# Kernel tuning notes

Hardware: AMD Instinct MI355X
Metric: run time of the kernel (lower is better)

## Reference

```python
import jax, jax.numpy as jnp
import numpy as np

TOP_K = 2
SCALING = 2.0  # LoRA alpha/rank scaling


def setup_inputs() -> dict:
    key = jax.random.key(0)
    ks = jax.random.split(key, 10)
    B, S, H, I, E, R = 1, 512, 2048, 1024, 8, 16
    w = 1.0 / np.sqrt(H)
    inp = {
        "x": jax.random.normal(ks[0], (B, S, H), jnp.float32),
        "gate_weight": jax.random.normal(ks[1], (E, H), jnp.float32) * w,
        "gate_lora_A": jax.random.normal(ks[2], (R, H), jnp.float32) * 0.02,
        "gate_lora_B": jax.random.normal(ks[3], (E, R), jnp.float32) * 0.02,
        "gate_up_proj": jax.random.normal(ks[4], (E, H, 2 * I), jnp.float32) * w,
        "down_proj": jax.random.normal(ks[5], (E, I, H), jnp.float32) * (1.0 / np.sqrt(I)),
        "gup_lora_A": jax.random.normal(ks[6], (E, R, H), jnp.float32) * 0.02,
        "gup_lora_B": jax.random.normal(ks[7], (E, 2 * I, R), jnp.float32) * 0.02,
        "down_lora_A": jax.random.normal(ks[8], (E, R, I), jnp.float32) * 0.02,
        "down_lora_B": jax.random.normal(ks[9], (E, H, R), jnp.float32) * 0.02,
    }
    return inp


def reference(x, gate_weight, gate_lora_A, gate_lora_B, gate_up_proj, down_proj,
              gup_lora_A, gup_lora_B, down_lora_A, down_lora_B):
    B, S, H = x.shape
    xf = x.reshape(-1, H)  # [T, H]

    # ---- router (base weight + LoRA delta) ----
    gate_delta = SCALING * (gate_lora_B @ gate_lora_A)  # [E, H]
    router_logits = xf @ gate_weight.T + xf @ gate_delta.T  # [T, E]
    probs = jax.nn.softmax(router_logits.astype(jnp.float32), axis=-1)
    routing_weights, selected = jax.lax.top_k(probs, TOP_K)  # [T, K]
    routing_weights = routing_weights / routing_weights.sum(-1, keepdims=True)  # norm_topk_prob
    routing_weights = routing_weights.astype(xf.dtype)

    # ---- expert MLP: compute all experts, combine top-k ----
    # (math identical to sparse scatter/grouped-GEMM dispatch for selected experts)
    gup = jnp.einsum('th,eho->teo', xf, gate_up_proj)  # [T, E, 2I]
    gup = gup + SCALING * jnp.einsum('ter,eor->teo',
                                     jnp.einsum('th,erh->ter', xf, gup_lora_A),
                                     gup_lora_B)
    gates, h = jnp.split(gup, 2, axis=-1)
    h = jax.nn.silu(gates) * h  # [T, E, I]

    out = jnp.einsum('tei,eih->teh', h, down_proj)  # [T, E, H]
    out = out + SCALING * jnp.einsum('ter,ehr->teh',
                                     jnp.einsum('tei,eri->ter', h, down_lora_A),
                                     down_lora_B)

    # gather the top-k expert outputs and combine with routing weights
    out_sel = jnp.take_along_axis(out, selected[:, :, None], axis=1)  # [T, K, H]
    y = jnp.einsum('tkh,tk->th', out_sel, routing_weights)
    return y.reshape(B, S, H)
```

## Files before the change

kernel.cpp:

```cpp
#include <hip/hip_runtime.h>


typedef short  s16x8 __attribute__((ext_vector_type(8)));
typedef float  f32x4 __attribute__((ext_vector_type(4)));
typedef unsigned short u16x8 __attribute__((ext_vector_type(8)));

__device__ __forceinline__ unsigned short f2bf(float f) {
  unsigned u = __builtin_bit_cast(unsigned, f);
  u += 0x7fffu + ((u >> 16) & 1u);
  return (unsigned short)(u >> 16);
}

#define PIPE_BARRIER() asm volatile("s_waitcnt lgkmcnt(0)\n\ts_barrier" ::: "memory")

#define OFF_CNT    0u
#define OFF_TER1A  256u
#define OFF_TER2   262400u
#define ZERO_SPAN  327936u
#define OFF_LIST   327936u
#define OFF_PW     344320u
#define OFF_WG     348416u
#define OFF_XBF    413952u
#define OFF_H      2511104u
#define OFF_OSEL   4608256u

__global__ void k_gatecomb(const float* __restrict__ gw, const float* __restrict__ gA,
                           const float* __restrict__ gB, float* __restrict__ Wg) {
  int idx = blockIdx.x * 256 + threadIdx.x;
  int e = idx >> 11, h = idx & 2047;
  float acc = gw[idx];
#pragma unroll
  for (int r = 0; r < 16; ++r)
    acc += 2.0f * gB[e * 16 + r] * gA[r * 2048 + h];
  Wg[idx] = acc;
}

__global__ void k_router(const float* __restrict__ x, const float* __restrict__ Wg,
                         int* __restrict__ cnt, int* __restrict__ list,
                         float* __restrict__ pw, unsigned short* __restrict__ xbf) {
  int t = blockIdx.x, tid = threadIdx.x;
  __shared__ float xs[2048];
  __shared__ float logits[8];
  for (int i = tid; i < 2048; i += 256) xs[i] = x[(size_t)t * 2048 + i];
  __syncthreads();
  {
    u16x8 o;
#pragma unroll
    for (int j = 0; j < 8; ++j) o[j] = f2bf(xs[tid * 8 + j]);
    *(u16x8*)(xbf + (size_t)t * 2048 + tid * 8) = o;
  }
  int e = tid >> 5, l = tid & 31;
  float s = 0.f;
  for (int h = l; h < 2048; h += 32) s += xs[h] * Wg[e * 2048 + h];
#pragma unroll
  for (int off = 16; off >= 1; off >>= 1) s += __shfl_down(s, off, 32);
  if (l == 0) logits[e] = s;
  __syncthreads();
  if (tid == 0) {
    float m = logits[0];
#pragma unroll
    for (int i = 1; i < 8; ++i) m = fmaxf(m, logits[i]);
    float ex[8];
#pragma unroll
    for (int i = 0; i < 8; ++i) ex[i] = __expf(logits[i] - m);
    int e1 = 0; float v1 = ex[0];
#pragma unroll
    for (int i = 1; i < 8; ++i) if (ex[i] > v1) { v1 = ex[i]; e1 = i; }
    int e2 = -1; float v2 = -1.f;
#pragma unroll
    for (int i = 0; i < 8; ++i) if (i != e1 && ex[i] > v2) { v2 = ex[i]; e2 = i; }
    float inv = 1.f / (v1 + v2);
    int p1 = 2 * t, p2 = 2 * t + 1;
    pw[p1] = v1 * inv;
    pw[p2] = v2 * inv;
    int s1 = atomicAdd(&cnt[e1], 1); list[e1 * 512 + s1] = p1;
    int s2 = atomicAdd(&cnt[e2], 1); list[e2 * 512 + s2] = p2;
  }
}

__global__ __launch_bounds__(512) void k_ter1all(
    const unsigned short* __restrict__ xbf, const float* __restrict__ gupA,
    float* __restrict__ ter1all) {
  int trow = blockIdx.x, kcc = blockIdx.y;
  int tid = threadIdx.x;
  __shared__ unsigned short Ap[2][64 * 64];
  __shared__ unsigned short Bp[2][128 * 64];
  const int k0b = kcc * 512;

  int rowA = tid >> 3, k16A = tid & 7;
  const unsigned short* aSrc = xbf + (size_t)(trow * 64 + rowA) * 2048 + k0b + k16A * 8;
  int aOff = rowA * 64 + ((k16A * 8) ^ ((rowA & 7) << 3));

  const float* bSrc[2]; int bOff[2];
#pragma unroll
  for (int s = 0; s < 2; ++s) {
    int slot = tid + s * 512;
    int er = slot >> 3, kg = slot & 7;
    bSrc[s] = gupA + (size_t)er * 2048 + k0b + kg * 8;
    bOff[s] = er * 64 + ((kg * 8) ^ ((er & 7) << 3));
  }
  int lane = tid & 63, wv = tid >> 6;
  int lr = lane & 15, lh = lane >> 4;

  uint4 apre; float4 bpre[2][2];
#define TA_ISSUE(T) { int kk = (T) * 64;                                   \
    apre = *(const uint4*)(aSrc + kk);                                     \
    _Pragma("unroll") for (int s = 0; s < 2; ++s) {                        \
      bpre[s][0] = *(const float4*)(bSrc[s] + kk);                         \
      bpre[s][1] = *(const float4*)(bSrc[s] + kk + 4); } }

  f32x4 acc[4] = {};
  TA_ISSUE(0);
  for (int t = 0; t < 8; ++t) {
    int buf = t & 1;
    *(uint4*)&Ap[buf][aOff] = apre;
#pragma unroll
    for (int s = 0; s < 2; ++s) {
      u16x8 o;
      o[0]=f2bf(bpre[s][0].x); o[1]=f2bf(bpre[s][0].y); o[2]=f2bf(bpre[s][0].z); o[3]=f2bf(bpre[s][0].w);
      o[4]=f2bf(bpre[s][1].x); o[5]=f2bf(bpre[s][1].y); o[6]=f2bf(bpre[s][1].z); o[7]=f2bf(bpre[s][1].w);
      *(u16x8*)&Bp[buf][bOff[s]] = o;
    }
    __syncthreads();
    if (t < 7) TA_ISSUE(t + 1);
#pragma unroll
    for (int ks = 0; ks < 64; ks += 32) {
      int kb = ks + lh * 8;
      int bc = wv * 16 + lr;
      s16x8 b = *(const s16x8*)&Bp[buf][bc * 64 + (kb ^ ((bc & 7) << 3))];
#pragma unroll
      for (int fr = 0; fr < 4; ++fr) {
        int ar = fr * 16 + lr;
        s16x8 a = *(const s16x8*)&Ap[buf][ar * 64 + (kb ^ ((ar & 7) << 3))];
        acc[fr] = __builtin_amdgcn_mfma_f32_16x16x32_bf16(a, b, acc[fr], 0, 0, 0);
      }
    }
    __syncthreads();
  }
#undef TA_ISSUE
#pragma unroll
  for (int fr = 0; fr < 4; ++fr)
#pragma unroll
    for (int j = 0; j < 4; ++j) {
      int tok = trow * 64 + fr * 16 + lh * 4 + j;
      atomicAdd(&ter1all[tok * 128 + wv * 16 + lr], acc[fr][j]);
    }
}

__global__ __launch_bounds__(512) void k_gemm1(
    const unsigned short* __restrict__ xbf, const float* __restrict__ gup,
    const float* __restrict__ gupB, const float* __restrict__ ter1all,
    const int* __restrict__ cnt, const int* __restrict__ list,
    unsigned short* __restrict__ h) {
  const int ct = blockIdx.x;
  const int st = blockIdx.y;
  const int e  = blockIdx.z;
  const int n = cnt[e];
  if (st * 128 >= n) return;
  const int tid = threadIdx.x;

  __shared__ unsigned short Ap[2][128 * 64];
  __shared__ unsigned short Bp[2][128 * 64];

  const int c0 = ct * 64;

  const unsigned short *aSrc0, *aSrc1;
  int aOff0, aOff1;
  {
    int row = tid >> 3, k16 = tid & 7;
    int p = list[e * 512 + min(st * 128 + row, n - 1)];
    aSrc0 = xbf + (size_t)(p >> 1) * 2048 + k16 * 8;
    aOff0 = row * 64 + ((k16 * 8) ^ ((row & 7) << 3));
    int slot = tid + 512;
    row = slot >> 3; k16 = slot & 7;
    p = list[e * 512 + min(st * 128 + row, n - 1)];
    aSrc1 = xbf + (size_t)(p >> 1) * 2048 + k16 * 8;
    aOff1 = row * 64 + ((k16 * 8) ^ ((row & 7) << 3));
  }
  const int bcol = tid & 127, kgrp = tid >> 7;
  const int gcg = (bcol < 64) ? (c0 + bcol) : (1024 + c0 + bcol - 64);
  const float* bSrc = gup + (size_t)e * 2048 * 2048 + (size_t)(kgrp * 16) * 2048 + gcg;
  const int sw = (bcol & 7) << 3;
  const int bOff0 = bcol * 64 + ((kgrp * 16) ^ sw);
  const int bOff1 = bcol * 64 + ((kgrp * 16 + 8) ^ sw);

  const int lane = tid & 63, wv = tid >> 6;
  const int lr = lane & 15, lh = lane >> 4;
  const int wr = wv >> 1, ni = wv & 1;

  uint4 a0A, a1A, a0B, a1B;
  float bA[16], bB[16];

#define G1_LOAD(SUF, T) {                                        \
    const int kk = (T) * 64;                                     \
    a0##SUF = *(const uint4*)(aSrc0 + kk);                       \
    a1##SUF = *(const uint4*)(aSrc1 + kk);                       \
    _Pragma("unroll") for (int j = 0; j < 16; ++j)               \
      b##SUF[j] = bSrc[(size_t)(kk + j) * 2048]; }

#define G1_BODY(BUF, SUF, NXT) {                                               \
    *(uint4*)&Ap[BUF][aOff0] = a0##SUF;                                        \
    *(uint4*)&Ap[BUF][aOff1] = a1##SUF;                                        \
    { u16x8 o0, o1;                                                            \
      _Pragma("unroll") for (int j = 0; j < 8; ++j) {                          \
        o0[j] = f2bf(b##SUF[j]); o1[j] = f2bf(b##SUF[j + 8]); }                \
      *(u16x8*)&Bp[BUF][bOff0] = o0;                                           \
      *(u16x8*)&Bp[BUF][bOff1] = o1; }                                         \
    PIPE_BARRIER();                                                            \
    if ((NXT) < 32) G1_LOAD(SUF, NXT);                                         \
    _Pragma("unroll") for (int ks = 0; ks < 64; ks += 32) {                    \
      int kb = ks + lh * 8;                                                    \
      s16x8 af[2], bg[2], bu[2];                                               \
      _Pragma("unroll") for (int q = 0; q < 2; ++q) {                          \
        int ar = wr * 32 + q * 16 + lr;                                        \
        af[q] = *(const s16x8*)&Ap[BUF][ar * 64 + (kb ^ ((ar & 7) << 3))];     \
      }                                                                        \
      _Pragma("unroll") for (int r = 0; r < 2; ++r) {                          \
        int bc = ni * 32 + r * 16 + lr;                                        \
        bg[r] = *(const s16x8*)&Bp[BUF][bc * 64 + (kb ^ ((bc & 7) << 3))];     \
        bu[r] = *(const s16x8*)&Bp[BUF][(bc + 64) * 64 + (kb ^ ((bc & 7) << 3))]; \
      }                                                                        \
      _Pragma("unroll") for (int q = 0; q < 2; ++q)                            \
        _Pragma("unroll") for (int r = 0; r < 2; ++r) {                        \
          accg[q][r] = __builtin_amdgcn_mfma_f32_16x16x32_bf16(af[q], bg[r], accg[q][r], 0, 0, 0); \
          accu[q][r] = __builtin_amdgcn_mfma_f32_16x16x32_bf16(af[q], bu[r], accu[q][r], 0, 0, 0); \
        }                                                                      \
    } }

  f32x4 accg[2][2] = {}, accu[2][2] = {};
  G1_LOAD(A, 0);
  G1_LOAD(B, 1);
  for (int tt = 0; tt < 32; tt += 2) {
    G1_BODY(0, A, tt + 2);
    G1_BODY(1, B, tt + 3);
  }
#undef G1_LOAD
#undef G1_BODY

  __syncthreads();
  float* tlds = (float*)&Ap[0][0];
  for (int idx = tid; idx < 2048; idx += 512) {
    int row = idx >> 4, c = idx & 15;
    int p = list[e * 512 + min(st * 128 + row, n - 1)];
    tlds[idx] = ter1all[(size_t)(p >> 1) * 128 + e * 16 + c];
  }
  __syncthreads();
#pragma unroll
  for (int r = 0; r < 2; ++r) {
    int gc = c0 + ni * 32 + r * 16 + lr;
    const float4* g4 = (const float4*)(gupB + ((size_t)e * 2048 + gc) * 16);
    const float4* u4 = (const float4*)(gupB + ((size_t)e * 2048 + 1024 + gc) * 16);
    float gv2[16], uv2[16];
#pragma unroll
    for (int q = 0; q < 4; ++q) {
      float4 gv = g4[q], uv = u4[q];
      gv2[q*4+0]=gv.x; gv2[q*4+1]=gv.y; gv2[q*4+2]=gv.z; gv2[q*4+3]=gv.w;
      uv2[q*4+0]=uv.x; uv2[q*4+1]=uv.y; uv2[q*4+2]=uv.z; uv2[q*4+3]=uv.w;
    }
#pragma unroll
    for (int q = 0; q < 2; ++q) {
#pragma unroll
      for (int j = 0; j < 4; ++j) {
        int row = wr * 32 + q * 16 + lh * 4 + j;
        if (st * 128 + row < n) {
          int p = list[e * 512 + st * 128 + row];
          const float* tv = &tlds[row * 16];
          float dg = 0.f, du = 0.f;
#pragma unroll
          for (int rr = 0; rr < 16; ++rr) { dg += tv[rr] * gv2[rr]; du += tv[rr] * uv2[rr]; }
          float g = accg[q][r][j] + 2.f * dg;
          float u = accu[q][r][j] + 2.f * du;
          h[(size_t)p * 1024 + gc] = f2bf(g / (1.f + __expf(-g)) * u);
        }
      }
    }
  }
}

__global__ __launch_bounds__(512) void k_ter2(
    const unsigned short* __restrict__ h, const float* __restrict__ dlA,
    const int* __restrict__ cnt, const int* __restrict__ list,
    float* __restrict__ ter2) {
  int st = blockIdx.x, kcc = blockIdx.y, e = blockIdx.z;
  int n = cnt[e];
  if (st * 128 >= n) return;
  int tid = threadIdx.x;
  __shared__ unsigned short Ap[2][128 * 64];
  __shared__ unsigned short Bp[2][16 * 64];
  const int k0b = kcc * 256;

  const unsigned short* aSrc[2]; int aOff[2];
#pragma unroll
  for (int s = 0; s < 2; ++s) {
    int slot = tid + s * 512;
    int row = slot >> 3, k16 = slot & 7;
    int p = list[e * 512 + min(st * 128 + row, n - 1)];
    aSrc[s] = h + (size_t)p * 1024 + k0b + k16 * 8;
    aOff[s] = row * 64 + ((k16 * 8) ^ ((row & 7) << 3));
  }
  const float* bSrc = nullptr; int bOff = 0;
  if (tid < 128) {
    int r = tid >> 3, kg = tid & 7;
    bSrc = dlA + ((size_t)e * 16 + r) * 1024 + k0b + kg * 8;
    bOff = r * 64 + ((kg * 8) ^ ((r & 7) << 3));
  }
  int lane = tid & 63, wv = tid >> 6;
  int lr = lane & 15, lh = lane >> 4;

  uint4 apre[2]; float4 bpre[2];
#define T2_ISSUE(T) { int kk = (T) * 64;                                   \
    _Pragma("unroll") for (int s = 0; s < 2; ++s)                          \
        apre[s] = *(const uint4*)(aSrc[s] + kk);                           \
    if (tid < 128) { bpre[0] = *(const float4*)(bSrc + kk);                \
                     bpre[1] = *(const float4*)(bSrc + kk + 4); } }

  f32x4 acc = {};
  T2_ISSUE(0);
  for (int t = 0; t < 4; ++t) {
    int buf = t & 1;
#pragma unroll
    for (int s = 0; s < 2; ++s) *(uint4*)&Ap[buf][aOff[s]] = apre[s];
    if (tid < 128) {
      u16x8 o;
      o[0]=f2bf(bpre[0].x); o[1]=f2bf(bpre[0].y); o[2]=f2bf(bpre[0].z); o[3]=f2bf(bpre[0].w);
      o[4]=f2bf(bpre[1].x); o[5]=f2bf(bpre[1].y); o[6]=f2bf(bpre[1].z); o[7]=f2bf(bpre[1].w);
      *(u16x8*)&Bp[buf][bOff] = o;
    }
    __syncthreads();
    if (t < 3) T2_ISSUE(t + 1);
#pragma unroll
    for (int ks = 0; ks < 64; ks += 32) {
      int kb = ks + lh * 8;
      s16x8 b = *(const s16x8*)&Bp[buf][lr * 64 + (kb ^ ((lr & 7) << 3))];
      int ar = wv * 16 + lr;
      s16x8 a = *(const s16x8*)&Ap[buf][ar * 64 + (kb ^ ((ar & 7) << 3))];
      acc = __builtin_amdgcn_mfma_f32_16x16x32_bf16(a, b, acc, 0, 0, 0);
    }
    __syncthreads();
  }
#undef T2_ISSUE
#pragma unroll
  for (int j = 0; j < 4; ++j) {
    int row = wv * 16 + lh * 4 + j;
    if (st * 128 + row < n) {
      int p = list[e * 512 + st * 128 + row];
      atomicAdd(&ter2[p * 16 + lr], acc[j]);
    }
  }
}

__global__ __launch_bounds__(512) void k_gemm2(
    const unsigned short* __restrict__ h, const float* __restrict__ down,
    const float* __restrict__ dlB, const float* __restrict__ ter2,
    const int* __restrict__ cnt, const int* __restrict__ list,
    float* __restrict__ osel) {
  const int ct = blockIdx.x;
  const int st = blockIdx.y;
  const int e  = blockIdx.z;
  const int n = cnt[e];
  if (st * 128 >= n) return;
  const int tid = threadIdx.x;

  __shared__ unsigned short Ap[2][128 * 64];
  __shared__ unsigned short Bp[2][64 * 64];

  const int c0 = ct * 64;

  const unsigned short *aSrc0, *aSrc1;
  int aOff0, aOff1;
  {
    int row = tid >> 3, k16 = tid & 7;
    int p = list[e * 512 + min(st * 128 + row, n - 1)];
    aSrc0 = h + (size_t)p * 1024 + k16 * 8;
    aOff0 = row * 64 + ((k16 * 8) ^ ((row & 7) << 3));
    int slot = tid + 512;
    row = slot >> 3; k16 = slot & 7;
    p = list[e * 512 + min(st * 128 + row, n - 1)];
    aSrc1 = h + (size_t)p * 1024 + k16 * 8;
    aOff1 = row * 64 + ((k16 * 8) ^ ((row & 7) << 3));
  }
  const int bcol = tid & 63, kg = tid >> 6;
  const float* bSrc = down + (size_t)e * 1024 * 2048 + (size_t)(kg * 8) * 2048 + c0 + bcol;
  const int bOff = bcol * 64 + ((kg * 8) ^ ((bcol & 7) << 3));

  const int lane = tid & 63, wv = tid >> 6;
  const int lr = lane & 15, lh = lane >> 4;
  const int wr = wv >> 1, ni = wv & 1;

  uint4 a0A, a1A, a0B, a1B;
  float bA[8], bB[8];

#define G2_LOAD(SUF, T) {                                        \
    const int kk = (T) * 64;                                     \
    a0##SUF = *(const uint4*)(aSrc0 + kk);                       \
    a1##SUF = *(const uint4*)(aSrc1 + kk);                       \
    _Pragma("unroll") for (int j = 0; j < 8; ++j)                \
      b##SUF[j] = bSrc[(size_t)(kk + j) * 2048]; }

#define G2_BODY(BUF, SUF, NXT) {                                               \
    *(uint4*)&Ap[BUF][aOff0] = a0##SUF;                                        \
    *(uint4*)&Ap[BUF][aOff1] = a1##SUF;                                        \
    { u16x8 o;                                                                 \
      _Pragma("unroll") for (int j = 0; j < 8; ++j) o[j] = f2bf(b##SUF[j]);    \
      *(u16x8*)&Bp[BUF][bOff] = o; }                                           \
    PIPE_BARRIER();                                                            \
    if ((NXT) < 16) G2_LOAD(SUF, NXT);                                         \
    _Pragma("unroll") for (int ks = 0; ks < 64; ks += 32) {                    \
      int kb = ks + lh * 8;                                                    \
      s16x8 af[2], bd[2];                                                      \
      _Pragma("unroll") for (int q = 0; q < 2; ++q) {                          \
        int ar = wr * 32 + q * 16 + lr;                                        \
        af[q] = *(const s16x8*)&Ap[BUF][ar * 64 + (kb ^ ((ar & 7) << 3))];     \
      }                                                                        \
      _Pragma("unroll") for (int r = 0; r < 2; ++r) {                          \
        int bc = ni * 32 + r * 16 + lr;                                        \
        bd[r] = *(const s16x8*)&Bp[BUF][bc * 64 + (kb ^ ((bc & 7) << 3))];     \
      }                                                                        \
      _Pragma("unroll") for (int q = 0; q < 2; ++q)                            \
        _Pragma("unroll") for (int r = 0; r < 2; ++r)                          \
          acc[q][r] = __builtin_amdgcn_mfma_f32_16x16x32_bf16(af[q], bd[r], acc[q][r], 0, 0, 0); \
    } }

  f32x4 acc[2][2] = {};
  G2_LOAD(A, 0);
  G2_LOAD(B, 1);
  for (int tt = 0; tt < 16; tt += 2) {
    G2_BODY(0, A, tt + 2);
    G2_BODY(1, B, tt + 3);
  }
#undef G2_LOAD
#undef G2_BODY

  __syncthreads();
  float* t2l = (float*)&Ap[0][0];
  for (int idx = tid; idx < 2048; idx += 512) {
    int row = idx >> 4, c = idx & 15;
    int p = list[e * 512 + min(st * 128 + row, n - 1)];
    t2l[idx] = ter2[p * 16 + c];
  }
  __syncthreads();
#pragma unroll
  for (int r = 0; r < 2; ++r) {
    int yc = c0 + ni * 32 + r * 16 + lr;
    const float4* d4 = (const float4*)(dlB + ((size_t)e * 2048 + yc) * 16);
    float d2[16];
#pragma unroll
    for (int q = 0; q < 4; ++q) {
      float4 v = d4[q];
      d2[q*4+0]=v.x; d2[q*4+1]=v.y; d2[q*4+2]=v.z; d2[q*4+3]=v.w;
    }
#pragma unroll
    for (int q = 0; q < 2; ++q) {
#pragma unroll
      for (int j = 0; j < 4; ++j) {
        int row = wr * 32 + q * 16 + lh * 4 + j;
        if (st * 128 + row < n) {
          int p = list[e * 512 + st * 128 + row];
          const float* tv = &t2l[row * 16];
          float dd = 0.f;
#pragma unroll
          for (int rr = 0; rr < 16; ++rr) dd += tv[rr] * d2[rr];
          osel[(size_t)p * 2048 + yc] = acc[q][r][j] + 2.f * dd;
        }
      }
    }
  }
}

__global__ __launch_bounds__(256) void k_comb(
    const float* __restrict__ osel, const float* __restrict__ pw,
    float* __restrict__ y) {
  int i = blockIdx.x * 256 + threadIdx.x;
  int t = i >> 9;
  int c4 = i & 511;
  float w1 = pw[2 * t], w2 = pw[2 * t + 1];
  const float4* o = (const float4*)osel;
  float4 a = o[(size_t)(2 * t) * 512 + c4];
  float4 b = o[(size_t)(2 * t + 1) * 512 + c4];
  float4 rv;
  rv.x = w1 * a.x + w2 * b.x;
  rv.y = w1 * a.y + w2 * b.y;
  rv.z = w1 * a.z + w2 * b.z;
  rv.w = w1 * a.w + w2 * b.w;
  ((float4*)y)[i] = rv;
}

extern "C" void kernel_launch(void* const* d_in, const int* in_sizes, int n_in,
                              void* d_out, int out_size, void* d_ws, size_t ws_size,
                              hipStream_t stream) {
  (void)in_sizes; (void)n_in; (void)ws_size; (void)out_size;
  const float* x    = (const float*)d_in[0];
  const float* gw   = (const float*)d_in[1];
  const float* gA   = (const float*)d_in[2];
  const float* gB   = (const float*)d_in[3];
  const float* gup  = (const float*)d_in[4];
  const float* down = (const float*)d_in[5];
  const float* gupA = (const float*)d_in[6];
  const float* gupB = (const float*)d_in[7];
  const float* dlA  = (const float*)d_in[8];
  const float* dlB  = (const float*)d_in[9];
  float* y = (float*)d_out;

  char* w = (char*)d_ws;
  int*   cnt           = (int*)(w + OFF_CNT);
  float* ter1all       = (float*)(w + OFF_TER1A);
  float* ter2          = (float*)(w + OFF_TER2);
  int*   list          = (int*)(w + OFF_LIST);
  float* pw            = (float*)(w + OFF_PW);
  float* Wg            = (float*)(w + OFF_WG);
  unsigned short* xbf  = (unsigned short*)(w + OFF_XBF);
  unsigned short* hbuf = (unsigned short*)(w + OFF_H);
  float* osel          = (float*)(w + OFF_OSEL);

  hipMemsetAsync(w, 0, ZERO_SPAN, stream);

  k_gatecomb<<<64, 256, 0, stream>>>(gw, gA, gB, Wg);
  k_router<<<512, 256, 0, stream>>>(x, Wg, cnt, list, pw, xbf);
  k_ter1all<<<dim3(8, 4), 512, 0, stream>>>(xbf, gupA, ter1all);
  k_gemm1<<<dim3(16, 4, 8), 512, 0, stream>>>(xbf, gup, gupB, ter1all, cnt, list, hbuf);
  k_ter2<<<dim3(4, 4, 8), 512, 0, stream>>>(hbuf, dlA, cnt, list, ter2);
  k_gemm2<<<dim3(32, 4, 8), 512, 0, stream>>>(hbuf, down, dlB, ter2, cnt, list, osel);
  k_comb<<<1024, 256, 0, stream>>>(osel, pw, y);
}
```

Baseline: 132.8 us.

## Halve GEMM column tiles, vectorize fp32 weight loads, interleave experts in flat grid

Both expert GEMMs now use 32-column tiles instead of 64, doubling the block count so more CUs stay busy given the uneven per-expert token counts. The grid is flattened with the expert index in the low bits, which spreads experts across consecutive blocks. The fp32 weight tiles are now read as row-contiguous float4 loads instead of strided scalar column loads, then converted and scattered into LDS. In exchange, each block does less MFMA work per A-tile load, so A (token activations) is re-read from global memory twice as often, and the LDS stores become narrower and more scattered.

```diff
diff --git a/kernel.cpp b/kernel.cpp
--- a/kernel.cpp
+++ b/kernel.cpp
@@ -3,6 +3,7 @@
 
 typedef short  s16x8 __attribute__((ext_vector_type(8)));
 typedef float  f32x4 __attribute__((ext_vector_type(4)));
+typedef unsigned short u16x4 __attribute__((ext_vector_type(4)));
 typedef unsigned short u16x8 __attribute__((ext_vector_type(8)));
 
 __device__ __forceinline__ unsigned short f2bf(float f) {
@@ -152,17 +153,19 @@
     const float* __restrict__ gupB, const float* __restrict__ ter1all,
     const int* __restrict__ cnt, const int* __restrict__ list,
     unsigned short* __restrict__ h) {
-  const int ct = blockIdx.x;
-  const int st = blockIdx.y;
-  const int e  = blockIdx.z;
+  const int id = blockIdx.x;
+  const int e  = id & 7;
+  const int m  = id >> 3;
+  const int ct = m & 31;
+  const int st = m >> 5;
   const int n = cnt[e];
   if (st * 128 >= n) return;
   const int tid = threadIdx.x;
 
   __shared__ unsigned short Ap[2][128 * 64];
-  __shared__ unsigned short Bp[2][128 * 64];
-
-  const int c0 = ct * 64;
+  __shared__ unsigned short Bp[2][64 * 64];
+
+  const int c0 = ct * 32;
 
   const unsigned short *aSrc0, *aSrc1;
   int aOff0, aOff1;
@@ -177,57 +180,56 @@
     aSrc1 = xbf + (size_t)(p >> 1) * 2048 + k16 * 8;
     aOff1 = row * 64 + ((k16 * 8) ^ ((row & 7) << 3));
   }
-  const int bcol = tid & 127, kgrp = tid >> 7;
-  const int gcg = (bcol < 64) ? (c0 + bcol) : (1024 + c0 + bcol - 64);
-  const float* bSrc = gup + (size_t)e * 2048 * 2048 + (size_t)(kgrp * 16) * 2048 + gcg;
-  const int sw = (bcol & 7) << 3;
-  const int bOff0 = bcol * 64 + ((kgrp * 16) ^ sw);
-  const int bOff1 = bcol * 64 + ((kgrp * 16 + 8) ^ sw);
+  const int c4 = (tid & 15) * 4;
+  const int kr2 = (tid >> 4) * 2;
+  const int gcol = (c4 < 32) ? (c0 + c4) : (1024 + c0 + c4 - 32);
+  const float* bSrc = gup + (size_t)e * 2048 * 2048 + (size_t)kr2 * 2048 + gcol;
+  int bOffc[4];
+#pragma unroll
+  for (int cc = 0; cc < 4; ++cc)
+    bOffc[cc] = (c4 + cc) * 64 + (kr2 ^ (((c4 + cc) & 7) << 3));
 
   const int lane = tid & 63, wv = tid >> 6;
   const int lr = lane & 15, lh = lane >> 4;
   const int wr = wv >> 1, ni = wv & 1;
 
   uint4 a0A, a1A, a0B, a1B;
-  float bA[16], bB[16];
-
-#define G1_LOAD(SUF, T) {                                        \
-    const int kk = (T) * 64;                                     \
-    a0##SUF = *(const uint4*)(aSrc0 + kk);                       \
-    a1##SUF = *(const uint4*)(aSrc1 + kk);                       \
-    _Pragma("unroll") for (int j = 0; j < 16; ++j)               \
-      b##SUF[j] = bSrc[(size_t)(kk + j) * 2048]; }
+  float bA[2][4], bB[2][4];
+
+#define G1_LOAD(SUF, T) {                                          \
+    const int kk = (T) * 64;                                       \
+    a0##SUF = *(const uint4*)(aSrc0 + kk);                         \
+    a1##SUF = *(const uint4*)(aSrc1 + kk);                         \
+    *(float4*)&b##SUF[0][0] = *(const float4*)(bSrc + (size_t)kk * 2048);        \
+    *(float4*)&b##SUF[1][0] = *(const float4*)(bSrc + (size_t)(kk + 1) * 2048); }
 
 #define G1_BODY(BUF, SUF, NXT) {                                               \
     *(uint4*)&Ap[BUF][aOff0] = a0##SUF;                                        \
     *(uint4*)&Ap[BUF][aOff1] = a1##SUF;                                        \
-    { u16x8 o0, o1;                                                            \
-      _Pragma("unroll") for (int j = 0; j < 8; ++j) {                          \
-        o0[j] = f2bf(b##SUF[j]); o1[j] = f2bf(b##SUF[j + 8]); }                \
-      *(u16x8*)&Bp[BUF][bOff0] = o0;                                           \
-      *(u16x8*)&Bp[BUF][bOff1] = o1; }                                         \
+    _Pragma("unroll") for (int cc = 0; cc < 4; ++cc) {                         \
+      unsigned o = (unsigned)f2bf(b##SUF[0][cc]) |                             \
+                   ((unsigned)f2bf(b##SUF[1][cc]) << 16);                      \
+      *(unsigned*)&Bp[BUF][bOffc[cc]] = o;                                     \
+    }                                                                          \
     PIPE_BARRIER();                                                            \
     if ((NXT) < 32) G1_LOAD(SUF, NXT);                                         \
     _Pragma("unroll") for (int ks = 0; ks < 64; ks += 32) {                    \
       int kb = ks + lh * 8;                                                    \
-      s16x8 af[2], bg[2], bu[2];                                               \
+      s16x8 af[2], bg, bu;                                                     \
       _Pragma("unroll") for (int q = 0; q < 2; ++q) {                          \
         int ar = wr * 32 + q * 16 + lr;                                        \
         af[q] = *(const s16x8*)&Ap[BUF][ar * 64 + (kb ^ ((ar & 7) << 3))];     \
       }                                                                        \
-      _Pragma("unroll") for (int r = 0; r < 2; ++r) {                          \
-        int bc = ni * 32 + r * 16 + lr;                                        \
-        bg[r] = *(const s16x8*)&Bp[BUF][bc * 64 + (kb ^ ((bc & 7) << 3))];     \
-        bu[r] = *(const s16x8*)&Bp[BUF][(bc + 64) * 64 + (kb ^ ((bc & 7) << 3))]; \
+      { int bc = ni * 16 + lr;                                                 \
+        bg = *(const s16x8*)&Bp[BUF][bc * 64 + (kb ^ ((bc & 7) << 3))];        \
+        bu = *(const s16x8*)&Bp[BUF][(bc + 32) * 64 + (kb ^ (((bc + 32) & 7) << 3))]; } \
+      _Pragma("unroll") for (int q = 0; q < 2; ++q) {                          \
+        accg[q] = __builtin_amdgcn_mfma_f32_16x16x32_bf16(af[q], bg, accg[q], 0, 0, 0); \
+        accu[q] = __builtin_amdgcn_mfma_f32_16x16x32_bf16(af[q], bu, accu[q], 0, 0, 0); \
       }                                                                        \
-      _Pragma("unroll") for (int q = 0; q < 2; ++q)                            \
-        _Pragma("unroll") for (int r = 0; r < 2; ++r) {                        \
-          accg[q][r] = __builtin_amdgcn_mfma_f32_16x16x32_bf16(af[q], bg[r], accg[q][r], 0, 0, 0); \
-          accu[q][r] = __builtin_amdgcn_mfma_f32_16x16x32_bf16(af[q], bu[r], accu[q][r], 0, 0, 0); \
-        }                                                                      \
     } }
 
-  f32x4 accg[2][2] = {}, accu[2][2] = {};
+  f32x4 accg[2] = {}, accu[2] = {};
   G1_LOAD(A, 0);
   G1_LOAD(B, 1);
   for (int tt = 0; tt < 32; tt += 2) {
@@ -245,9 +247,8 @@
     tlds[idx] = ter1all[(size_t)(p >> 1) * 128 + e * 16 + c];
   }
   __syncthreads();
-#pragma unroll
-  for (int r = 0; r < 2; ++r) {
-    int gc = c0 + ni * 32 + r * 16 + lr;
+  {
+    int gc = c0 + ni * 16 + lr;
     const float4* g4 = (const float4*)(gupB + ((size_t)e * 2048 + gc) * 16);
     const float4* u4 = (const float4*)(gupB + ((size_t)e * 2048 + 1024 + gc) * 16);
     float gv2[16], uv2[16];
@@ -268,8 +269,8 @@
           float dg = 0.f, du = 0.f;
 #pragma unroll
           for (int rr = 0; rr < 16; ++rr) { dg += tv[rr] * gv2[rr]; du += tv[rr] * uv2[rr]; }
-          float g = accg[q][r][j] + 2.f * dg;
-          float u = accu[q][r][j] + 2.f * du;
+          float g = accg[q][j] + 2.f * dg;
+          float u = accu[q][j] + 2.f * du;
           h[(size_t)p * 1024 + gc] = f2bf(g / (1.f + __expf(-g)) * u);
         }
       }
@@ -354,17 +355,19 @@
     const float* __restrict__ dlB, const float* __restrict__ ter2,
     const int* __restrict__ cnt, const int* __restrict__ list,
     float* __restrict__ osel) {
-  const int ct = blockIdx.x;
-  const int st = blockIdx.y;
-  const int e  = blockIdx.z;
+  const int id = blockIdx.x;
+  const int e  = id & 7;
+  const int m  = id >> 3;
+  const int ct = m & 63;
+  const int st = m >> 6;
   const int n = cnt[e];
   if (st * 128 >= n) return;
   const int tid = threadIdx.x;
 
   __shared__ unsigned short Ap[2][128 * 64];
-  __shared__ unsigned short Bp[2][64 * 64];
-
-  const int c0 = ct * 64;
+  __shared__ unsigned short Bp[2][32 * 64];
+
+  const int c0 = ct * 32;
 
   const unsigned short *aSrc0, *aSrc1;
   int aOff0, aOff1;
@@ -379,49 +382,48 @@
     aSrc1 = h + (size_t)p * 1024 + k16 * 8;
     aOff1 = row * 64 + ((k16 * 8) ^ ((row & 7) << 3));
   }
-  const int bcol = tid & 63, kg = tid >> 6;
-  const float* bSrc = down + (size_t)e * 1024 * 2048 + (size_t)(kg * 8) * 2048 + c0 + bcol;
-  const int bOff = bcol * 64 + ((kg * 8) ^ ((bcol & 7) << 3));
+  const int c4 = (tid & 7) * 4;
+  const int kr = tid >> 3;
+  const float* bSrc = down + ((size_t)e * 1024 + kr) * 2048 + c0 + c4;
+  int bOffc[4];
+#pragma unroll
+  for (int cc = 0; cc < 4; ++cc)
+    bOffc[cc] = (c4 + cc) * 64 + (kr ^ (((c4 + cc) & 7) << 3));
 
   const int lane = tid & 63, wv = tid >> 6;
   const int lr = lane & 15, lh = lane >> 4;
   const int wr = wv >> 1, ni = wv & 1;
 
   uint4 a0A, a1A, a0B, a1B;
-  float bA[8], bB[8];
-
-#define G2_LOAD(SUF, T) {                                        \
-    const int kk = (T) * 64;                                     \
-    a0##SUF = *(const uint4*)(aSrc0 + kk);                       \
-    a1##SUF = *(const uint4*)(aSrc1 + kk);                       \
-    _Pragma("unroll") for (int j = 0; j < 8; ++j)                \
-      b##SUF[j] = bSrc[(size_t)(kk + j) * 2048]; }
+  float bA[4], bB[4];
+
+#define G2_LOAD(SUF, T) {                                          \
+    const int kk = (T) * 64;                                       \
+    a0##SUF = *(const uint4*)(aSrc0 + kk);                         \
+    a1##SUF = *(const uint4*)(aSrc1 + kk);                         \
+    *(float4*)&b##SUF[0] = *(const float4*)(bSrc + (size_t)kk * 2048); }
 
 #define G2_BODY(BUF, SUF, NXT) {                                               \
     *(uint4*)&Ap[BUF][aOff0] = a0##SUF;                                        \
     *(uint4*)&Ap[BUF][aOff1] = a1##SUF;                                        \
-    { u16x8 o;                                                                 \
-      _Pragma("unroll") for (int j = 0; j < 8; ++j) o[j] = f2bf(b##SUF[j]);    \
-      *(u16x8*)&Bp[BUF][bOff] = o; }                                           \
+    _Pragma("unroll") for (int cc = 0; cc < 4; ++cc)                           \
+      Bp[BUF][bOffc[cc]] = f2bf(b##SUF[cc]);                                   \
     PIPE_BARRIER();                                                            \
     if ((NXT) < 16) G2_LOAD(SUF, NXT);                                         \
     _Pragma("unroll") for (int ks = 0; ks < 64; ks += 32) {                    \
       int kb = ks + lh * 8;                                                    \
-      s16x8 af[2], bd[2];                                                      \
+      s16x8 af[2], bd;                                                         \
       _Pragma("unroll") for (int q = 0; q < 2; ++q) {                          \
         int ar = wr * 32 + q * 16 + lr;                                        \
         af[q] = *(const s16x8*)&Ap[BUF][ar * 64 + (kb ^ ((ar & 7) << 3))];     \
       }                                                                        \
-      _Pragma("unroll") for (int r = 0; r < 2; ++r) {                          \
-        int bc = ni * 32 + r * 16 + lr;                                        \
-        bd[r] = *(const s16x8*)&Bp[BUF][bc * 64 + (kb ^ ((bc & 7) << 3))];     \
-      }                                                                        \
+      { int bc = ni * 16 + lr;                                                 \
+        bd = *(const s16x8*)&Bp[BUF][bc * 64 + (kb ^ ((bc & 7) << 3))]; }      \
       _Pragma("unroll") for (int q = 0; q < 2; ++q)                            \
-        _Pragma("unroll") for (int r = 0; r < 2; ++r)                          \
-          acc[q][r] = __builtin_amdgcn_mfma_f32_16x16x32_bf16(af[q], bd[r], acc[q][r], 0, 0, 0); \
+        acc[q] = __builtin_amdgcn_mfma_f32_16x16x32_bf16(af[q], bd, acc[q], 0, 0, 0); \
     } }
 
-  f32x4 acc[2][2] = {};
+  f32x4 acc[2] = {};
   G2_LOAD(A, 0);
   G2_LOAD(B, 1);
   for (int tt = 0; tt < 16; tt += 2) {
@@ -439,9 +441,8 @@
     t2l[idx] = ter2[p * 16 + c];
   }
   __syncthreads();
-#pragma unroll
-  for (int r = 0; r < 2; ++r) {
-    int yc = c0 + ni * 32 + r * 16 + lr;
+  {
+    int yc = c0 + ni * 16 + lr;
     const float4* d4 = (const float4*)(dlB + ((size_t)e * 2048 + yc) * 16);
     float d2[16];
 #pragma unroll
@@ -460,7 +461,7 @@
           float dd = 0.f;
 #pragma unroll
           for (int rr = 0; rr < 16; ++rr) dd += tv[rr] * d2[rr];
-          osel[(size_t)p * 2048 + yc] = acc[q][r][j] + 2.f * dd;
+          osel[(size_t)p * 2048 + yc] = acc[q][j] + 2.f * dd;
         }
       }
     }
@@ -517,8 +518,8 @@
   k_gatecomb<<<64, 256, 0, stream>>>(gw, gA, gB, Wg);
   k_router<<<512, 256, 0, stream>>>(x, Wg, cnt, list, pw, xbf);
   k_ter1all<<<dim3(8, 4), 512, 0, stream>>>(xbf, gupA, ter1all);
-  k_gemm1<<<dim3(16, 4, 8), 512, 0, stream>>>(xbf, gup, gupB, ter1all, cnt, list, hbuf);
+  k_gemm1<<<1024, 512, 0, stream>>>(xbf, gup, gupB, ter1all, cnt, list, hbuf);
   k_ter2<<<dim3(4, 4, 8), 512, 0, stream>>>(hbuf, dlA, cnt, list, ter2);
-  k_gemm2<<<dim3(32, 4, 8), 512, 0, stream>>>(hbuf, down, dlB, ter2, cnt, list, osel);
+  k_gemm2<<<2048, 512, 0, stream>>>(hbuf, down, dlB, ter2, cnt, list, osel);
   k_comb<<<1024, 256, 0, stream>>>(osel, pw, y);
 }
```

Result: slower. 138.4 us (+4.2%).
